# Kernel tuning notes

Hardware: AMD Instinct MI355X
Metric: run time of the kernel (lower is better)

Reference implementation:

```python
import jax, jax.numpy as jnp
import numpy as np

B, S, EMB, H = 4, 1024, 1024, 16
HD = EMB // H          # head_dim = 64
MAXP = 512             # RelativePositionalEncoder default max_position


def setup_inputs() -> dict:
    key = jax.random.key(0)
    ks = jax.random.split(key, 13)
    s = 1.0 / np.sqrt(EMB)  # xavier-ish scale keeps softmax logits sane
    return {
        "query": jax.random.normal(ks[0], (B, S, EMB), jnp.float32),
        "key": jax.random.normal(ks[1], (B, S, EMB), jnp.float32),
        "value": jax.random.normal(ks[2], (B, S, EMB), jnp.float32),
        "Wq": jax.random.normal(ks[3], (EMB, EMB), jnp.float32) * s,
        "bq": jnp.zeros((EMB,), jnp.float32),
        "Wk": jax.random.normal(ks[4], (EMB, EMB), jnp.float32) * s,
        "bk": jnp.zeros((EMB,), jnp.float32),
        "Wv": jax.random.normal(ks[5], (EMB, EMB), jnp.float32) * s,
        "bv": jnp.zeros((EMB,), jnp.float32),
        "Wo": jax.random.normal(ks[6], (EMB, EMB), jnp.float32) * s,
        "bo": jnp.zeros((EMB,), jnp.float32),
        "rel_k": jax.random.normal(ks[7], (2 * MAXP + 1, HD), jnp.float32) * 0.05,
        "rel_v": jax.random.normal(ks[8], (2 * MAXP + 1, HD), jnp.float32) * 0.05,
    }


def _split_heads(x):
    # [B,S,E] -> [B,S,H,HD] -> [B,H,S,HD] -> [B*H,S,HD]
    return x.reshape(B, S, H, HD).transpose(0, 2, 1, 3).reshape(B * H, S, HD)


def reference(query, key, value, Wq, bq, Wk, bk, Wv, bv, Wo, bo, rel_k, rel_v):
    scale = jnp.sqrt(jnp.asarray(HD, query.dtype))
    q = _split_heads(query @ Wq + bq)
    k = _split_heads(key @ Wk + bk)
    v = _split_heads(value @ Wv + bv)
    # relative position lookup tables: [Sq, Sk, HD]
    rp = jnp.clip(jnp.arange(S)[None, :] - jnp.arange(S)[:, None], -MAXP, MAXP) + MAXP
    a_key = rel_k[rp]
    a_value = rel_v[rp]
    qk = jnp.einsum('bqd,bkd->bqk', q, k)              # [B*H,S,S]
    rel_qk = jnp.einsum('bqd,qkd->bqk', q, a_key)      # relative score term
    attn = jax.nn.softmax((qk + rel_qk) / scale, axis=-1)
    out = jnp.einsum('bqk,bkd->bqd', attn, v) + jnp.einsum('bqk,qkd->bqd', attn, a_value)
    # faithful to original's view(num_heads, batch, -1, head_dim) then concat reshape
    out = out.reshape(H, B, S, HD).transpose(0, 2, 1, 3).reshape(B, S, H * HD)
    out = out @ Wo + bo
    return (out, attn)
```

## Files before the change

kernel.cpp:

```cpp
#include <hip/hip_runtime.h>


using s16x8 = __attribute__((ext_vector_type(8))) short;
using f32x4 = __attribute__((ext_vector_type(4))) float;

#define MFMA16 __builtin_amdgcn_mfma_f32_16x16x32_bf16

__device__ __forceinline__ float bf2f(unsigned short u) {
  union { unsigned int u; float f; } v; v.u = ((unsigned int)u) << 16; return v.f;
}
__device__ __forceinline__ unsigned short f2bf(float f) {
  union { float f; unsigned int u; } v; v.f = f;
  unsigned int r = (v.u + 0x7FFFu + ((v.u >> 16) & 1u)) >> 16;
  return (unsigned short)r;
}

__global__ __launch_bounds__(256)
void k_prep(const float* __restrict__ Wq, const float* __restrict__ Wk,
            const float* __restrict__ Wv, const float* __restrict__ Wo,
            unsigned short* __restrict__ wqt, unsigned short* __restrict__ wkt,
            unsigned short* __restrict__ wvt, unsigned short* __restrict__ wot,
            const float* __restrict__ rk, const float* __restrict__ rv,
            unsigned short* __restrict__ relkb, unsigned short* __restrict__ rvTb) {
  const int b = blockIdx.x;
  const int tid = threadIdx.x;
  if (b < 4096) {
    __shared__ float t[32][33];
    const int sel = b >> 10, idx = b & 1023;
    const float* W = sel == 0 ? Wq : (sel == 1 ? Wk : (sel == 2 ? Wv : Wo));
    unsigned short* Wt = sel == 0 ? wqt : (sel == 1 ? wkt : (sel == 2 ? wvt : wot));
    const int n0 = (idx & 31) * 32, k0 = (idx >> 5) * 32;
    const int tx = tid & 31, ty = tid >> 5;
#pragma unroll
    for (int r = 0; r < 4; ++r)
      t[ty * 4 + r][tx] = W[(size_t)(k0 + ty * 4 + r) * 1024 + n0 + tx];
    __syncthreads();
#pragma unroll
    for (int r = 0; r < 4; ++r)
      Wt[(size_t)(n0 + ty * 4 + r) * 1024 + k0 + tx] = f2bf(t[tx][ty * 4 + r]);
  } else {
    const int b2 = b - 4096;
    if (b2 < 33) {
      int i = (b2 * 256 + tid) * 8;
      if (i < 65600) {
        float4 a = *(const float4*)(rk + i);
        float4 c = *(const float4*)(rk + i + 4);
        s16x8 o;
        o[0] = (short)f2bf(a.x); o[1] = (short)f2bf(a.y); o[2] = (short)f2bf(a.z); o[3] = (short)f2bf(a.w);
        o[4] = (short)f2bf(c.x); o[5] = (short)f2bf(c.y); o[6] = (short)f2bf(c.z); o[7] = (short)f2bf(c.w);
        *(s16x8*)(relkb + i) = o;
      }
    } else {
      int i = (b2 - 33) * 256 + tid;
      if (i < 65600) {
        int p = i >> 6, d = i & 63;
        rvTb[d * 1040 + p] = f2bf(rv[i]);
      }
    }
  }
}

__global__ __launch_bounds__(256)
void k_trV(const unsigned short* __restrict__ v, unsigned short* __restrict__ vt) {
  __shared__ unsigned short T[64][72];
  const int tid = threadIdx.x;
  const int bh = blockIdx.x >> 4;
  const int s0 = (blockIdx.x & 15) << 6;
  const int r = tid >> 2, cb = (tid & 3) << 4;
  const unsigned short* src = v + ((size_t)bh << 16) + (size_t)(s0 + r) * 64 + cb;
  *(s16x8*)&T[r][cb] = *(const s16x8*)src;
  *(s16x8*)&T[r][cb + 8] = *(const s16x8*)(src + 8);
  __syncthreads();
  unsigned short* dst = vt + ((size_t)bh << 16) + (size_t)r * 1024 + s0 + cb;
  s16x8 o0, o1;
#pragma unroll
  for (int e = 0; e < 8; ++e) o0[e] = T[cb + e][r];
#pragma unroll
  for (int e = 0; e < 8; ++e) o1[e] = T[cb + 8 + e][r];
  *(s16x8*)dst = o0;
  *(s16x8*)(dst + 8) = o1;
}

__global__ __launch_bounds__(256, 2)
void k_gemm_qkv(const float* __restrict__ Aq, const float* __restrict__ Ak, const float* __restrict__ Av,
                const unsigned short* __restrict__ Wq_, const unsigned short* __restrict__ Wk_,
                const unsigned short* __restrict__ Wv_,
                const float* __restrict__ bq_, const float* __restrict__ bk_, const float* __restrict__ bv_,
                unsigned short* __restrict__ Oq, unsigned short* __restrict__ Ok,
                unsigned short* __restrict__ Ov) {
  const int z = blockIdx.z;
  const float* A = z == 0 ? Aq : (z == 1 ? Ak : Av);
  const unsigned short* BT = z == 0 ? Wq_ : (z == 1 ? Wk_ : Wv_);
  const float* bias = z == 0 ? bq_ : (z == 1 ? bk_ : bv_);
  unsigned short* Cout = z == 0 ? Oq : (z == 1 ? Ok : Ov);

  __shared__ alignas(16) unsigned short aT[2][4096];
  __shared__ alignas(16) unsigned short bT[2][2048];
  const int tid = threadIdx.x;
  const int lane = tid & 63;
  const int l15 = lane & 15, lhi = lane >> 4;
  const int w = tid >> 6;
  const int wr = w * 32;
  const int brow = blockIdx.y * 128, bcol = blockIdx.x * 64;
  f32x4 acc[2][4] = {};

  const int c1 = tid, c2 = tid + 256;
  const int r1 = c1 >> 2, kA1 = (c1 & 3) * 8;
  const int r2 = c2 >> 2, kA2 = (c2 & 3) * 8;
  float4 a0, a1, a2, a3;
  s16x8 w1v, w2v;

#define LOADA(kt) do {                                                     \
    const float* p1 = A + (size_t)(brow + r1) * 1024 + (kt) * 32 + kA1;    \
    a0 = *(const float4*)p1; a1 = *(const float4*)(p1 + 4);                \
    const float* p2 = A + (size_t)(brow + r2) * 1024 + (kt) * 32 + kA2;    \
    a2 = *(const float4*)p2; a3 = *(const float4*)(p2 + 4);                \
  } while (0)
#define CVTA() do {                                                        \
    w1v[0] = (short)f2bf(a0.x); w1v[1] = (short)f2bf(a0.y);                \
    w1v[2] = (short)f2bf(a0.z); w1v[3] = (short)f2bf(a0.w);                \
    w1v[4] = (short)f2bf(a1.x); w1v[5] = (short)f2bf(a1.y);                \
    w1v[6] = (short)f2bf(a1.z); w1v[7] = (short)f2bf(a1.w);                \
    w2v[0] = (short)f2bf(a2.x); w2v[1] = (short)f2bf(a2.y);                \
    w2v[2] = (short)f2bf(a2.z); w2v[3] = (short)f2bf(a2.w);                \
    w2v[4] = (short)f2bf(a3.x); w2v[5] = (short)f2bf(a3.y);                \
    w2v[6] = (short)f2bf(a3.z); w2v[7] = (short)f2bf(a3.w);                \
  } while (0)
#define WRA(buf) do {                                                      \
    *(s16x8*)&aT[buf][c1 * 8] = w1v;                                       \
    *(s16x8*)&aT[buf][c2 * 8] = w2v;                                       \
  } while (0)
#define GLB(buf, kt) do {                                                  \
    int row = c1 >> 2, k8 = (c1 & 3) * 8;                                  \
    __builtin_amdgcn_global_load_lds(                                      \
      (const __attribute__((address_space(1))) void*)(BT + (size_t)(bcol + row) * 1024 + (kt) * 32 + k8), \
      (__attribute__((address_space(3))) void*)(&bT[buf][c1 * 8]), 16, 0, 0); \
  } while (0)

  LOADA(0); GLB(0, 0); CVTA(); WRA(0);
  int cur = 0;
  for (int kt = 0; kt < 32; ++kt) {
    __syncthreads();
    if (kt + 1 < 32) { LOADA(kt + 1); GLB(cur ^ 1, kt + 1); }
    s16x8 af[2], bfv[4];
#pragma unroll
    for (int m = 0; m < 2; ++m)
      af[m] = *(const s16x8*)&aT[cur][(wr + m * 16 + l15) * 32 + lhi * 8];
#pragma unroll
    for (int n = 0; n < 4; ++n)
      bfv[n] = *(const s16x8*)&bT[cur][(n * 16 + l15) * 32 + lhi * 8];
#pragma unroll
    for (int m = 0; m < 2; ++m)
#pragma unroll
      for (int n = 0; n < 4; ++n)
        acc[m][n] = MFMA16(af[m], bfv[n], acc[m][n], 0, 0, 0);
    if (kt + 1 < 32) { CVTA(); WRA(cur ^ 1); }
    __syncthreads();
    cur ^= 1;
  }
#undef LOADA
#undef CVTA
#undef WRA
#undef GLB

#pragma unroll
  for (int m = 0; m < 2; ++m) {
#pragma unroll
    for (int n = 0; n < 4; ++n) {
      int col = bcol + n * 16 + l15;
      float bs = bias[col];
#pragma unroll
      for (int j = 0; j < 4; ++j) {
        int r = brow + wr + m * 16 + lhi * 4 + j;
        float v = acc[m][n][j] + bs;
        int bb = r >> 10, s = r & 1023, h = col >> 6, d = col & 63;
        Cout[(((size_t)((bb << 4) + h) * 1024 + s) << 6) + d] = f2bf(v);
      }
    }
  }
}

__global__ __launch_bounds__(256, 2)
void k_gemm_o(const unsigned short* __restrict__ A, const unsigned short* __restrict__ BT,
              const float* __restrict__ bias, float* __restrict__ Cout) {
  __shared__ alignas(16) unsigned short aT[2][4096];
  __shared__ alignas(16) unsigned short bT[2][2048];
  const int tid = threadIdx.x;
  const int lane = tid & 63;
  const int l15 = lane & 15, lhi = lane >> 4;
  const int w = tid >> 6;
  const int wr = w * 32;
  const int brow = blockIdx.y * 128, bcol = blockIdx.x * 64;
  f32x4 acc[2][4] = {};

#define STAGE(buf, kt) do {                                                              \
    int k0s = (kt) * 32;                                                                 \
    {                                                                                    \
      int c = tid;                                                                       \
      int row = c >> 2, k8 = (c & 3) * 8;                                                \
      __builtin_amdgcn_global_load_lds(                                                  \
        (const __attribute__((address_space(1))) void*)(A + (size_t)(brow + row) * 1024 + k0s + k8), \
        (__attribute__((address_space(3))) void*)(&aT[buf][c * 8]), 16, 0, 0);           \
      __builtin_amdgcn_global_load_lds(                                                  \
        (const __attribute__((address_space(1))) void*)(BT + (size_t)(bcol + row) * 1024 + k0s + k8),\
        (__attribute__((address_space(3))) void*)(&bT[buf][c * 8]), 16, 0, 0);           \
    }                                                                                    \
    {                                                                                    \
      int c = tid + 256;                                                                 \
      int row = c >> 2, k8 = (c & 3) * 8;                                                \
      __builtin_amdgcn_global_load_lds(                                                  \
        (const __attribute__((address_space(1))) void*)(A + (size_t)(brow + row) * 1024 + k0s + k8), \
        (__attribute__((address_space(3))) void*)(&aT[buf][c * 8]), 16, 0, 0);           \
    }                                                                                    \
  } while (0)

  int cur = 0;
  STAGE(0, 0);
  for (int kt = 0; kt < 32; ++kt) {
    __syncthreads();
    if (kt + 1 < 32) STAGE(cur ^ 1, kt + 1);
    s16x8 af[2], bfv[4];
#pragma unroll
    for (int m = 0; m < 2; ++m)
      af[m] = *(const s16x8*)&aT[cur][(wr + m * 16 + l15) * 32 + lhi * 8];
#pragma unroll
    for (int n = 0; n < 4; ++n)
      bfv[n] = *(const s16x8*)&bT[cur][(n * 16 + l15) * 32 + lhi * 8];
#pragma unroll
    for (int m = 0; m < 2; ++m)
#pragma unroll
      for (int n = 0; n < 4; ++n)
        acc[m][n] = MFMA16(af[m], bfv[n], acc[m][n], 0, 0, 0);
    __syncthreads();
    cur ^= 1;
  }
#undef STAGE

#pragma unroll
  for (int m = 0; m < 2; ++m) {
#pragma unroll
    for (int n = 0; n < 4; ++n) {
      int col = bcol + n * 16 + l15;
      float bs = bias[col];
#pragma unroll
      for (int j = 0; j < 4; ++j) {
        int r = brow + wr + m * 16 + lhi * 4 + j;
        Cout[(size_t)r * 1024 + col] = acc[m][n][j] + bs;
      }
    }
  }
}

#define RPW 1032
#define PWP 520

__global__ __launch_bounds__(256, 3)
void k_attn(const unsigned short* __restrict__ qb, const unsigned short* __restrict__ kbm,
            const unsigned short* __restrict__ vT, const unsigned short* __restrict__ relk,
            const unsigned short* __restrict__ rvT, float* __restrict__ attn_out,
            unsigned short* __restrict__ xscr) {
  __shared__ alignas(16) unsigned short pbuf[16 * RPW];
  __shared__ alignas(16) unsigned short TbPw[16 * PWP];
  __shared__ float red[4][16];
  __shared__ float izS[16], plS[16], phS[16];

  const int tid = threadIdx.x;
  const int lane = tid & 63;
  const int w = tid >> 6;
  const int l15 = lane & 15, lhi = lane >> 4;
  const int orig = ((blockIdx.x & 7) << 9) | (blockIdx.x >> 3);
  const int bh = orig >> 6;
  const int q0 = (orig & 63) << 4;

  const unsigned short* Qh = qb + ((size_t)bh << 16);
  const unsigned short* Kh = kbm + ((size_t)bh << 16);
  const unsigned short* Vth = vT + ((size_t)bh << 16);

  const unsigned short* qp = Qh + (size_t)(q0 + l15) * 64 + lhi * 8;
  s16x8 qa0 = *(const s16x8*)qp;
  s16x8 qa1 = *(const s16x8*)(qp + 32);

  float zp = 0.f;
  for (int half = 0; half < 2; ++half) {
    const int khalf = half << 9;
    __syncthreads();

    {
      const int PT0 = ((khalf - q0 + 497) >> 4) << 4;
      const int PT1 = khalf - q0 + 1023;
      for (int pt = PT0 + w * 16; pt <= PT1; pt += 64) {
        int pr = pt + l15; pr = pr < 0 ? 0 : (pr > 1024 ? 1024 : pr);
        const unsigned short* rp = relk + (size_t)pr * 64 + lhi * 8;
        s16x8 rf0 = *(const s16x8*)rp;
        s16x8 rf1 = *(const s16x8*)(rp + 32);
        f32x4 d = {0.f, 0.f, 0.f, 0.f};
        d = MFMA16(qa0, rf0, d, 0, 0, 0);
        d = MFMA16(qa1, rf1, d, 0, 0, 0);
#pragma unroll
        for (int j = 0; j < 4; ++j) {
          int qi = lhi * 4 + j;
          int u = pt + l15 - khalf + q0 + qi - 512;
          if (u >= 0 && u < 512) TbPw[qi * PWP + u] = f2bf(d[j]);
        }
      }
    }
    __syncthreads();

    const unsigned short* kbp = Kh + (size_t)(khalf + w * 16 + l15) * 64 + lhi * 8;
#pragma unroll
    for (int g = 0; g < 2; ++g) {
      s16x8 kf0[4], kf1[4];
#pragma unroll
      for (int n = 0; n < 4; ++n) {
        const unsigned short* p = kbp + (size_t)(g * 4 + n) * 4096;
        kf0[n] = *(const s16x8*)p;
        kf1[n] = *(const s16x8*)(p + 32);
      }
#pragma unroll
      for (int n = 0; n < 4; ++n) {
        const int ktile = khalf + w * 16 + (g * 4 + n) * 64;
        f32x4 c = {0.f, 0.f, 0.f, 0.f};
        __builtin_amdgcn_s_setprio(1);
        c = MFMA16(kf0[n], qa0, c, 0, 0, 0);
        c = MFMA16(kf1[n], qa1, c, 0, 0, 0);
        __builtin_amdgcn_s_setprio(0);
        uint2 tv = *(const uint2*)&TbPw[l15 * PWP + (ktile - khalf) + lhi * 4];
        float t0 = bf2f((unsigned short)(tv.x & 0xFFFF));
        float t1 = bf2f((unsigned short)(tv.x >> 16));
        float t2 = bf2f((unsigned short)(tv.y & 0xFFFF));
        float t3 = bf2f((unsigned short)(tv.y >> 16));
        float e0 = __expf((c[0] + t0) * 0.125f);
        float e1 = __expf((c[1] + t1) * 0.125f);
        float e2 = __expf((c[2] + t2) * 0.125f);
        float e3 = __expf((c[3] + t3) * 0.125f);
        zp += (e0 + e1) + (e2 + e3);
        uint2 pk;
        pk.x = (unsigned int)f2bf(e0) | ((unsigned int)f2bf(e1) << 16);
        pk.y = (unsigned int)f2bf(e2) | ((unsigned int)f2bf(e3) << 16);
        *(uint2*)&pbuf[l15 * RPW + ktile + lhi * 4] = pk;
      }
    }
  }

  zp += __shfl_xor(zp, 16, 64);
  zp += __shfl_xor(zp, 32, 64);
  if (lane < 16) red[w][lane] = zp;
  __syncthreads();
  if (tid < 16)
    izS[tid] = 1.0f / (red[0][tid] + red[1][tid] + red[2][tid] + red[3][tid]);

  {
    const int qi = tid >> 4, tq = tid & 15;
    const int qa = q0 + qi;
    int lo, hi;
    const bool isPh = (qa < 512);
    if (isPh) { lo = qa + 512; hi = 1024; }
    else      { lo = 0;        hi = qa - 511; }
    float s = 0.f;
    const unsigned short* srow = pbuf + qi * RPW;
    const int kb0 = lo & ~7;
    for (int k8 = kb0 + tq * 8; k8 < hi; k8 += 128) {
      s16x8 v8 = *(const s16x8*)&srow[k8];
#pragma unroll
      for (int e = 0; e < 8; ++e) {
        int k = k8 + e;
        s += (k >= lo && k < hi) ? bf2f((unsigned short)v8[e]) : 0.f;
      }
    }
#pragma unroll
    for (int off = 1; off < 16; off <<= 1) s += __shfl_xor(s, off, 64);
    if (tq == 0) { plS[qi] = isPh ? 0.f : s; phS[qi] = isPh ? s : 0.f; }
  }
  __syncthreads();

  {
    float* ao = attn_out + ((size_t)bh << 20) + ((size_t)q0 << 10);
#pragma unroll
    for (int n = 0; n < 8; ++n) {
      int row = (tid >> 7) + n * 2;
      int c8 = (tid & 127) << 3;
      float iz = izS[row];
      s16x8 p8 = *(const s16x8*)&pbuf[row * RPW + c8];
      f32x4 o0, o1;
      o0[0] = bf2f((unsigned short)p8[0]) * iz; o0[1] = bf2f((unsigned short)p8[1]) * iz;
      o0[2] = bf2f((unsigned short)p8[2]) * iz; o0[3] = bf2f((unsigned short)p8[3]) * iz;
      o1[0] = bf2f((unsigned short)p8[4]) * iz; o1[1] = bf2f((unsigned short)p8[5]) * iz;
      o1[2] = bf2f((unsigned short)p8[6]) * iz; o1[3] = bf2f((unsigned short)p8[7]) * iz;
      __builtin_nontemporal_store(o0, (f32x4*)(ao + (row << 10) + c8));
      __builtin_nontemporal_store(o1, (f32x4*)(ao + (row << 10) + c8 + 4));
    }
  }

  f32x4 acc = {0.f, 0.f, 0.f, 0.f};
  const int d0w = w << 4;
  const unsigned short* vrow = Vth + (size_t)(d0w + l15) * 1024 + lhi * 8;
#pragma unroll 8
  for (int kc = 0; kc < 1024; kc += 32) {
    s16x8 pa = *(const s16x8*)&pbuf[l15 * RPW + kc + lhi * 8];
    s16x8 vf = *(const s16x8*)(vrow + kc);
    acc = MFMA16(pa, vf, acc, 0, 0, 0);
  }

  const unsigned short* rrow = rvT + (size_t)(d0w + l15) * 1040 + lhi * 8;
  {
    const int sqi = tid >> 4, stq = tid & 15;
    const int ssh = sqi & 7, shs = ssh >> 1;
    const bool sodd = (ssh & 1) != 0;
    unsigned short* drow = TbPw + sqi * PWP;
    const unsigned short* srow = pbuf + sqi * RPW;
    for (int ph = 0; ph < 2; ++ph) {
      __syncthreads();
      const int base = q0 + sqi + (ph ? 0 : -512);
      for (int t = stq; t < 64; t += 16) {
        const int kw0 = base + t * 8;
        s16x8 o;
        if (kw0 >= 0 && kw0 + 8 <= 1024) {
          const int A = kw0 - ssh;
          union { s16x8 v; unsigned int u[4]; } a0u, a1u, ov;
          a0u.v = *(const s16x8*)&srow[A];
          a1u.v = *(const s16x8*)&srow[A + 8];
          unsigned int wd[8];
#pragma unroll
          for (int j2 = 0; j2 < 4; ++j2) { wd[j2] = a0u.u[j2]; wd[4 + j2] = a1u.u[j2]; }
          unsigned int v7[7];
#pragma unroll
          for (int j2 = 0; j2 < 7; ++j2) {
            unsigned int sf = (wd[j2] >> 16) | (wd[j2 + 1] << 16);
            v7[j2] = sodd ? sf : wd[j2];
          }
#pragma unroll
          for (int j2 = 0; j2 < 4; ++j2) {
            unsigned int t0 = (shs & 1) ? v7[j2 + 1] : v7[j2];
            unsigned int t1 = (shs & 1) ? v7[j2 + 3] : v7[j2 + 2];
            ov.u[j2] = (shs & 2) ? t1 : t0;
          }
          o = ov.v;
        } else if (kw0 + 8 <= 0 || kw0 >= 1024) {
          o = (s16x8){0, 0, 0, 0, 0, 0, 0, 0};
        } else {
#pragma unroll
          for (int e = 0; e < 8; ++e) {
            int k = kw0 + e;
            int kc2 = k < 0 ? 0 : (k > 1023 ? 1023 : k);
            unsigned short vv = srow[kc2];
            o[e] = (k >= 0 && k < 1024) ? (short)vv : (short)0;
          }
        }
        *(s16x8*)&drow[t * 8] = o;
        if (ph == 0 && t == 0) drow[0] = f2bf(plS[sqi]);
      }
      __syncthreads();
#pragma unroll 8
      for (int kc = 0; kc < 512; kc += 32) {
        s16x8 pa = *(const s16x8*)&TbPw[l15 * PWP + kc + lhi * 8];
        s16x8 rb = *(const s16x8*)(rrow + (ph << 9) + kc);
        acc = MFMA16(pa, rb, acc, 0, 0, 0);
      }
    }
  }

  float rv1024 = bf2f(rvT[(size_t)(d0w + l15) * 1040 + 1024]);
  const size_t fb = ((size_t)(bh >> 2) << 18) + ((size_t)(bh & 3) << 6);
#pragma unroll
  for (int j = 0; j < 4; ++j) {
    int qi = lhi * 4 + j;
    float v = (acc[j] + phS[qi] * rv1024) * izS[qi];
    xscr[fb + ((size_t)(q0 + qi) << 8) + d0w + l15] = f2bf(v);
  }
}

extern "C" void kernel_launch(void* const* d_in, const int* in_sizes, int n_in,
                              void* d_out, int out_size, void* d_ws, size_t ws_size,
                              hipStream_t stream) {
  (void)in_sizes; (void)n_in; (void)out_size; (void)ws_size;
  const float* query = (const float*)d_in[0];
  const float* key   = (const float*)d_in[1];
  const float* value = (const float*)d_in[2];
  const float* Wq = (const float*)d_in[3];
  const float* bq = (const float*)d_in[4];
  const float* Wk = (const float*)d_in[5];
  const float* bk = (const float*)d_in[6];
  const float* Wv = (const float*)d_in[7];
  const float* bv = (const float*)d_in[8];
  const float* Wo = (const float*)d_in[9];
  const float* bo = (const float*)d_in[10];
  const float* rel_k = (const float*)d_in[11];
  const float* rel_v = (const float*)d_in[12];

  char* ws = (char*)d_ws;
  const size_t MB = 1024 * 1024;
  unsigned short* qb    = (unsigned short*)(ws);
  unsigned short* kbuf  = (unsigned short*)(ws + 8 * MB);
  unsigned short* vbuf  = (unsigned short*)(ws + 16 * MB);
  unsigned short* vTb   = (unsigned short*)(ws + 24 * MB);
  unsigned short* wqt   = (unsigned short*)(ws + 32 * MB);
  unsigned short* wkt   = (unsigned short*)(ws + 34 * MB);
  unsigned short* wvt   = (unsigned short*)(ws + 36 * MB);
  unsigned short* wot   = (unsigned short*)(ws + 38 * MB);
  unsigned short* relkb = (unsigned short*)(ws + 40 * MB);
  unsigned short* rvTb  = (unsigned short*)(ws + 40 * MB + 256 * 1024);
  unsigned short* xscr  = vbuf;

  float* out0 = (float*)d_out;
  float* attn_out = out0 + 4194304;

  k_prep<<<4386, 256, 0, stream>>>(Wq, Wk, Wv, Wo, wqt, wkt, wvt, wot,
                                   rel_k, rel_v, relkb, rvTb);

  k_gemm_qkv<<<dim3(16, 32, 3), 256, 0, stream>>>(query, key, value,
                                                  wqt, wkt, wvt,
                                                  bq, bk, bv,
                                                  qb, kbuf, vbuf);

  k_trV<<<1024, 256, 0, stream>>>(vbuf, vTb);

  k_attn<<<4096, 256, 0, stream>>>(qb, kbuf, vTb, relkb, rvTb, attn_out, xscr);

  k_gemm_o<<<dim3(16, 32), 256, 0, stream>>>(xscr, wot, bo, out0);
}
```

Baseline: 338.8 us.

## Fuse V transpose into QKV GEMM and shrink attention LDS footprint

The V projection epilogue now writes its output directly in transposed [bh][d][s] layout, which removes the separate transpose kernel and its extra pass over V. The attention kernel processes keys in eight 128-wide windows, so the relative-key staging buffer shrinks from 16x520 to 16x136. The rel_v term is now computed by building the shifted probability fragments in registers per MFMA step rather than through a staged LDS buffer with extra barriers. The P·V product is moved ahead of the attn output write. Lower LDS use allows launch bounds to rise to 4 blocks per CU, at the cost of more loop iterations and barriers in the score phase.

```diff
diff --git a/kernel.cpp b/kernel.cpp
--- a/kernel.cpp
+++ b/kernel.cpp
@@ -58,27 +58,6 @@
       }
     }
   }
-}
-
-__global__ __launch_bounds__(256)
-void k_trV(const unsigned short* __restrict__ v, unsigned short* __restrict__ vt) {
-  __shared__ unsigned short T[64][72];
-  const int tid = threadIdx.x;
-  const int bh = blockIdx.x >> 4;
-  const int s0 = (blockIdx.x & 15) << 6;
-  const int r = tid >> 2, cb = (tid & 3) << 4;
-  const unsigned short* src = v + ((size_t)bh << 16) + (size_t)(s0 + r) * 64 + cb;
-  *(s16x8*)&T[r][cb] = *(const s16x8*)src;
-  *(s16x8*)&T[r][cb + 8] = *(const s16x8*)(src + 8);
-  __syncthreads();
-  unsigned short* dst = vt + ((size_t)bh << 16) + (size_t)r * 1024 + s0 + cb;
-  s16x8 o0, o1;
-#pragma unroll
-  for (int e = 0; e < 8; ++e) o0[e] = T[cb + e][r];
-#pragma unroll
-  for (int e = 0; e < 8; ++e) o1[e] = T[cb + 8 + e][r];
-  *(s16x8*)dst = o0;
-  *(s16x8*)(dst + 8) = o1;
 }
 
 __global__ __launch_bounds__(256, 2)
@@ -163,18 +142,37 @@
 #undef WRA
 #undef GLB
 
-#pragma unroll
-  for (int m = 0; m < 2; ++m) {
-#pragma unroll
-    for (int n = 0; n < 4; ++n) {
-      int col = bcol + n * 16 + l15;
-      float bs = bias[col];
-#pragma unroll
-      for (int j = 0; j < 4; ++j) {
-        int r = brow + wr + m * 16 + lhi * 4 + j;
-        float v = acc[m][n][j] + bs;
-        int bb = r >> 10, s = r & 1023, h = col >> 6, d = col & 63;
-        Cout[(((size_t)((bb << 4) + h) * 1024 + s) << 6) + d] = f2bf(v);
+  if (z < 2) {
+#pragma unroll
+    for (int m = 0; m < 2; ++m) {
+#pragma unroll
+      for (int n = 0; n < 4; ++n) {
+        int col = bcol + n * 16 + l15;
+        float bs = bias[col];
+#pragma unroll
+        for (int j = 0; j < 4; ++j) {
+          int r = brow + wr + m * 16 + lhi * 4 + j;
+          float v = acc[m][n][j] + bs;
+          int bb = r >> 10, s = r & 1023, h = col >> 6, d = col & 63;
+          Cout[(((size_t)((bb << 4) + h) * 1024 + s) << 6) + d] = f2bf(v);
+        }
+      }
+    }
+  } else {
+    const int h = bcol >> 6;
+#pragma unroll
+    for (int m = 0; m < 2; ++m) {
+      int r0 = brow + wr + m * 16 + lhi * 4;
+      int bb = r0 >> 10, s0 = r0 & 1023;
+#pragma unroll
+      for (int n = 0; n < 4; ++n) {
+        int col = bcol + n * 16 + l15;
+        int d = col & 63;
+        float bs = bias[col];
+        uint2 pk;
+        pk.x = (unsigned int)f2bf(acc[m][n][0] + bs) | ((unsigned int)f2bf(acc[m][n][1] + bs) << 16);
+        pk.y = (unsigned int)f2bf(acc[m][n][2] + bs) | ((unsigned int)f2bf(acc[m][n][3] + bs) << 16);
+        *(uint2*)&Cout[(((size_t)((bb << 4) + h) << 16)) + (d << 10) + s0] = pk;
       }
     }
   }
@@ -252,15 +250,15 @@
 }
 
 #define RPW 1032
-#define PWP 520
-
-__global__ __launch_bounds__(256, 3)
+#define TBW 136
+
+__global__ __launch_bounds__(256, 4)
 void k_attn(const unsigned short* __restrict__ qb, const unsigned short* __restrict__ kbm,
             const unsigned short* __restrict__ vT, const unsigned short* __restrict__ relk,
             const unsigned short* __restrict__ rvT, float* __restrict__ attn_out,
             unsigned short* __restrict__ xscr) {
   __shared__ alignas(16) unsigned short pbuf[16 * RPW];
-  __shared__ alignas(16) unsigned short TbPw[16 * PWP];
+  __shared__ alignas(16) unsigned short Tb[16 * TBW];
   __shared__ float red[4][16];
   __shared__ float izS[16], plS[16], phS[16];
 
@@ -281,13 +279,14 @@
   s16x8 qa1 = *(const s16x8*)(qp + 32);
 
   float zp = 0.f;
-  for (int half = 0; half < 2; ++half) {
-    const int khalf = half << 9;
+#pragma unroll 1
+  for (int win = 0; win < 8; ++win) {
+    const int kw = win << 7;
     __syncthreads();
 
     {
-      const int PT0 = ((khalf - q0 + 497) >> 4) << 4;
-      const int PT1 = khalf - q0 + 1023;
+      const int PT0 = ((kw - q0 + 497) >> 4) << 4;
+      const int PT1 = kw - q0 + 639;
       for (int pt = PT0 + w * 16; pt <= PT1; pt += 64) {
         int pr = pt + l15; pr = pr < 0 ? 0 : (pr > 1024 ? 1024 : pr);
         const unsigned short* rp = relk + (size_t)pr * 64 + lhi * 8;
@@ -299,46 +298,42 @@
 #pragma unroll
         for (int j = 0; j < 4; ++j) {
           int qi = lhi * 4 + j;
-          int u = pt + l15 - khalf + q0 + qi - 512;
-          if (u >= 0 && u < 512) TbPw[qi * PWP + u] = f2bf(d[j]);
+          int u = pt + l15 - kw + q0 + qi - 512;
+          if (u >= 0 && u < 128) Tb[qi * TBW + u] = f2bf(d[j]);
         }
       }
     }
     __syncthreads();
 
-    const unsigned short* kbp = Kh + (size_t)(khalf + w * 16 + l15) * 64 + lhi * 8;
-#pragma unroll
-    for (int g = 0; g < 2; ++g) {
-      s16x8 kf0[4], kf1[4];
-#pragma unroll
-      for (int n = 0; n < 4; ++n) {
-        const unsigned short* p = kbp + (size_t)(g * 4 + n) * 4096;
-        kf0[n] = *(const s16x8*)p;
-        kf1[n] = *(const s16x8*)(p + 32);
-      }
-#pragma unroll
-      for (int n = 0; n < 4; ++n) {
-        const int ktile = khalf + w * 16 + (g * 4 + n) * 64;
-        f32x4 c = {0.f, 0.f, 0.f, 0.f};
-        __builtin_amdgcn_s_setprio(1);
-        c = MFMA16(kf0[n], qa0, c, 0, 0, 0);
-        c = MFMA16(kf1[n], qa1, c, 0, 0, 0);
-        __builtin_amdgcn_s_setprio(0);
-        uint2 tv = *(const uint2*)&TbPw[l15 * PWP + (ktile - khalf) + lhi * 4];
-        float t0 = bf2f((unsigned short)(tv.x & 0xFFFF));
-        float t1 = bf2f((unsigned short)(tv.x >> 16));
-        float t2 = bf2f((unsigned short)(tv.y & 0xFFFF));
-        float t3 = bf2f((unsigned short)(tv.y >> 16));
-        float e0 = __expf((c[0] + t0) * 0.125f);
-        float e1 = __expf((c[1] + t1) * 0.125f);
-        float e2 = __expf((c[2] + t2) * 0.125f);
-        float e3 = __expf((c[3] + t3) * 0.125f);
-        zp += (e0 + e1) + (e2 + e3);
-        uint2 pk;
-        pk.x = (unsigned int)f2bf(e0) | ((unsigned int)f2bf(e1) << 16);
-        pk.y = (unsigned int)f2bf(e2) | ((unsigned int)f2bf(e3) << 16);
-        *(uint2*)&pbuf[l15 * RPW + ktile + lhi * 4] = pk;
-      }
+    const unsigned short* kbp = Kh + (size_t)(kw + w * 16 + l15) * 64 + lhi * 8;
+    s16x8 kf0a = *(const s16x8*)kbp;
+    s16x8 kf1a = *(const s16x8*)(kbp + 32);
+    s16x8 kf0b = *(const s16x8*)(kbp + 4096);
+    s16x8 kf1b = *(const s16x8*)(kbp + 4096 + 32);
+#pragma unroll
+    for (int n = 0; n < 2; ++n) {
+      const int ktile = kw + w * 16 + n * 64;
+      s16x8 kf0 = n ? kf0b : kf0a;
+      s16x8 kf1 = n ? kf1b : kf1a;
+      f32x4 c = {0.f, 0.f, 0.f, 0.f};
+      __builtin_amdgcn_s_setprio(1);
+      c = MFMA16(kf0, qa0, c, 0, 0, 0);
+      c = MFMA16(kf1, qa1, c, 0, 0, 0);
+      __builtin_amdgcn_s_setprio(0);
+      uint2 tv = *(const uint2*)&Tb[l15 * TBW + (ktile - kw) + lhi * 4];
+      float t0 = bf2f((unsigned short)(tv.x & 0xFFFF));
+      float t1 = bf2f((unsigned short)(tv.x >> 16));
+      float t2 = bf2f((unsigned short)(tv.y & 0xFFFF));
+      float t3 = bf2f((unsigned short)(tv.y >> 16));
+      float e0 = __expf((c[0] + t0) * 0.125f);
+      float e1 = __expf((c[1] + t1) * 0.125f);
+      float e2 = __expf((c[2] + t2) * 0.125f);
+      float e3 = __expf((c[3] + t3) * 0.125f);
+      zp += (e0 + e1) + (e2 + e3);
+      uint2 pk;
+      pk.x = (unsigned int)f2bf(e0) | ((unsigned int)f2bf(e1) << 16);
+      pk.y = (unsigned int)f2bf(e2) | ((unsigned int)f2bf(e3) << 16);
+      *(uint2*)&pbuf[l15 * RPW + ktile + lhi * 4] = pk;
     }
   }
 
@@ -373,6 +368,16 @@
   }
   __syncthreads();
 
+  f32x4 acc = {0.f, 0.f, 0.f, 0.f};
+  const int d0w = w << 4;
+  const unsigned short* vrow = Vth + (size_t)(d0w + l15) * 1024 + lhi * 8;
+#pragma unroll 8
+  for (int kc = 0; kc < 1024; kc += 32) {
+    s16x8 pa = *(const s16x8*)&pbuf[l15 * RPW + kc + lhi * 8];
+    s16x8 vf = *(const s16x8*)(vrow + kc);
+    acc = MFMA16(pa, vf, acc, 0, 0, 0);
+  }
+
   {
     float* ao = attn_out + ((size_t)bh << 20) + ((size_t)q0 << 10);
 #pragma unroll
@@ -391,72 +396,51 @@
     }
   }
 
-  f32x4 acc = {0.f, 0.f, 0.f, 0.f};
-  const int d0w = w << 4;
-  const unsigned short* vrow = Vth + (size_t)(d0w + l15) * 1024 + lhi * 8;
-#pragma unroll 8
-  for (int kc = 0; kc < 1024; kc += 32) {
-    s16x8 pa = *(const s16x8*)&pbuf[l15 * RPW + kc + lhi * 8];
-    s16x8 vf = *(const s16x8*)(vrow + kc);
-    acc = MFMA16(pa, vf, acc, 0, 0, 0);
-  }
-
   const unsigned short* rrow = rvT + (size_t)(d0w + l15) * 1040 + lhi * 8;
-  {
-    const int sqi = tid >> 4, stq = tid & 15;
-    const int ssh = sqi & 7, shs = ssh >> 1;
-    const bool sodd = (ssh & 1) != 0;
-    unsigned short* drow = TbPw + sqi * PWP;
-    const unsigned short* srow = pbuf + sqi * RPW;
-    for (int ph = 0; ph < 2; ++ph) {
-      __syncthreads();
-      const int base = q0 + sqi + (ph ? 0 : -512);
-      for (int t = stq; t < 64; t += 16) {
-        const int kw0 = base + t * 8;
-        s16x8 o;
-        if (kw0 >= 0 && kw0 + 8 <= 1024) {
-          const int A = kw0 - ssh;
-          union { s16x8 v; unsigned int u[4]; } a0u, a1u, ov;
-          a0u.v = *(const s16x8*)&srow[A];
-          a1u.v = *(const s16x8*)&srow[A + 8];
-          unsigned int wd[8];
-#pragma unroll
-          for (int j2 = 0; j2 < 4; ++j2) { wd[j2] = a0u.u[j2]; wd[4 + j2] = a1u.u[j2]; }
-          unsigned int v7[7];
-#pragma unroll
-          for (int j2 = 0; j2 < 7; ++j2) {
-            unsigned int sf = (wd[j2] >> 16) | (wd[j2 + 1] << 16);
-            v7[j2] = sodd ? sf : wd[j2];
-          }
-#pragma unroll
-          for (int j2 = 0; j2 < 4; ++j2) {
-            unsigned int t0 = (shs & 1) ? v7[j2 + 1] : v7[j2];
-            unsigned int t1 = (shs & 1) ? v7[j2 + 3] : v7[j2 + 2];
-            ov.u[j2] = (shs & 2) ? t1 : t0;
-          }
-          o = ov.v;
-        } else if (kw0 + 8 <= 0 || kw0 >= 1024) {
-          o = (s16x8){0, 0, 0, 0, 0, 0, 0, 0};
-        } else {
-#pragma unroll
-          for (int e = 0; e < 8; ++e) {
-            int k = kw0 + e;
-            int kc2 = k < 0 ? 0 : (k > 1023 ? 1023 : k);
-            unsigned short vv = srow[kc2];
-            o[e] = (k >= 0 && k < 1024) ? (short)vv : (short)0;
-          }
-        }
-        *(s16x8*)&drow[t * 8] = o;
-        if (ph == 0 && t == 0) drow[0] = f2bf(plS[sqi]);
-      }
-      __syncthreads();
-#pragma unroll 8
-      for (int kc = 0; kc < 512; kc += 32) {
-        s16x8 pa = *(const s16x8*)&TbPw[l15 * PWP + kc + lhi * 8];
-        s16x8 rb = *(const s16x8*)(rrow + (ph << 9) + kc);
-        acc = MFMA16(pa, rb, acc, 0, 0, 0);
-      }
-    }
+  const float pl = plS[l15];
+  const int ssh = l15 & 7, shs = ssh >> 1;
+  const bool sodd = (ssh & 1) != 0;
+  const unsigned short* srow = pbuf + l15 * RPW;
+  for (int uc = 0; uc < 1024; uc += 32) {
+    if (uc + 79 + q0 <= 512) continue;
+    if (uc + q0 >= 1536) break;
+    const int base = q0 + l15 + uc + lhi * 8 - 512;
+    s16x8 wa;
+    if (base >= 8 && base <= 1008) {
+      const int A = base - ssh;
+      union { s16x8 v; unsigned int u[4]; } a0u, a1u, ov;
+      a0u.v = *(const s16x8*)&srow[A];
+      a1u.v = *(const s16x8*)&srow[A + 8];
+      unsigned int wd[8];
+#pragma unroll
+      for (int j2 = 0; j2 < 4; ++j2) { wd[j2] = a0u.u[j2]; wd[4 + j2] = a1u.u[j2]; }
+      unsigned int v7[7];
+#pragma unroll
+      for (int j2 = 0; j2 < 7; ++j2) {
+        unsigned int sf = (wd[j2] >> 16) | (wd[j2 + 1] << 16);
+        v7[j2] = sodd ? sf : wd[j2];
+      }
+#pragma unroll
+      for (int j2 = 0; j2 < 4; ++j2) {
+        unsigned int t0 = (shs & 1) ? v7[j2 + 1] : v7[j2];
+        unsigned int t1 = (shs & 1) ? v7[j2 + 3] : v7[j2 + 2];
+        ov.u[j2] = (shs & 2) ? t1 : t0;
+      }
+      wa = ov.v;
+    } else if (base + 8 <= 0 || base >= 1024) {
+      wa = (s16x8){0, 0, 0, 0, 0, 0, 0, 0};
+    } else {
+#pragma unroll
+      for (int e = 0; e < 8; ++e) {
+        int k = base + e;
+        int kc2 = k < 0 ? 0 : (k > 1023 ? 1023 : k);
+        unsigned short vv = srow[kc2];
+        wa[e] = (k >= 0 && k < 1024) ? (short)vv : (short)0;
+      }
+    }
+    if (uc == 0 && lhi == 0) wa[0] = (short)f2bf(pl);
+    s16x8 rb = *(const s16x8*)(rrow + uc);
+    acc = MFMA16(wa, rb, acc, 0, 0, 0);
   }
 
   float rv1024 = bf2f(rvT[(size_t)(d0w + l15) * 1040 + 1024]);
@@ -491,7 +475,7 @@
   const size_t MB = 1024 * 1024;
   unsigned short* qb    = (unsigned short*)(ws);
   unsigned short* kbuf  = (unsigned short*)(ws + 8 * MB);
-  unsigned short* vbuf  = (unsigned short*)(ws + 16 * MB);
+  unsigned short* xscr  = (unsigned short*)(ws + 16 * MB);
   unsigned short* vTb   = (unsigned short*)(ws + 24 * MB);
   unsigned short* wqt   = (unsigned short*)(ws + 32 * MB);
   unsigned short* wkt   = (unsigned short*)(ws + 34 * MB);
@@ -499,7 +483,6 @@
   unsigned short* wot   = (unsigned short*)(ws + 38 * MB);
   unsigned short* relkb = (unsigned short*)(ws + 40 * MB);
   unsigned short* rvTb  = (unsigned short*)(ws + 40 * MB + 256 * 1024);
-  unsigned short* xscr  = vbuf;
 
   float* out0 = (float*)d_out;
   float* attn_out = out0 + 4194304;
@@ -510,9 +493,7 @@
   k_gemm_qkv<<<dim3(16, 32, 3), 256, 0, stream>>>(query, key, value,
                                                   wqt, wkt, wvt,
                                                   bq, bk, bv,
-                                                  qb, kbuf, vbuf);
-
-  k_trV<<<1024, 256, 0, stream>>>(vbuf, vTb);
+                                                  qb, kbuf, vTb);
 
   k_attn<<<4096, 256, 0, stream>>>(qb, kbuf, vTb, relkb, rvTb, attn_out, xscr);
 
```

New measurement: 450.4 us. 1.33x slower.
